# Optimization experiments

Measured on AMD Instinct MI355X. Metric: run time of the kernel, lower is better.

Reference implementation:

```python
import jax, jax.numpy as jnp
import numpy as np

HIDDEN = 1024
NUM_HEADS = 16
DK = 64  # key_and_query_dim
DV = 64  # value_dim
NEG_INF = -1.0e9


def setup_inputs() -> dict:
    key = jax.random.key(0)
    ks = jax.random.split(key, 12)
    B, S = 4, 2048
    scale = 0.02
    return {
        "q_hidden_inputs": jax.random.normal(ks[0], (B, S, HIDDEN), dtype=jnp.float32),
        "k_hidden_inputs": jax.random.normal(ks[1], (B, S, HIDDEN), dtype=jnp.float32),
        "v_hidden_inputs": jax.random.normal(ks[2], (B, S, HIDDEN), dtype=jnp.float32),
        "mask": jax.random.randint(ks[3], (B, S, S), 0, 2) > 0,
        # per-head projection weights, stacked over heads: [H, hidden, dk/dv]
        "wq": jax.random.normal(ks[4], (NUM_HEADS, HIDDEN, DK), dtype=jnp.float32) * scale,
        "bq": jax.random.normal(ks[5], (NUM_HEADS, DK), dtype=jnp.float32) * scale,
        "wk": jax.random.normal(ks[6], (NUM_HEADS, HIDDEN, DK), dtype=jnp.float32) * scale,
        "bk": jax.random.normal(ks[7], (NUM_HEADS, DK), dtype=jnp.float32) * scale,
        "wv": jax.random.normal(ks[8], (NUM_HEADS, HIDDEN, DV), dtype=jnp.float32) * scale,
        "bv": jax.random.normal(ks[9], (NUM_HEADS, DV), dtype=jnp.float32) * scale,
        # output projection: [H*dv, hidden]
        "wo": jax.random.normal(ks[10], (NUM_HEADS * DV, HIDDEN), dtype=jnp.float32) * scale,
        "bo": jax.random.normal(ks[11], (HIDDEN,), dtype=jnp.float32) * scale,
    }


def reference(q_hidden_inputs, k_hidden_inputs, v_hidden_inputs, mask,
              wq, bq, wk, bk, wv, bv, wo, bo):
    # Per-head linear projections, vectorized over heads: [B, H, S, dk]
    q = jnp.einsum('bsd,hdk->bhsk', q_hidden_inputs, wq) + bq[None, :, None, :]
    k = jnp.einsum('bsd,hdk->bhsk', k_hidden_inputs, wk) + bk[None, :, None, :]
    v = jnp.einsum('bsd,hdv->bhsv', v_hidden_inputs, wv) + bv[None, :, None, :]
    # scores: [B, H, Sq, Sk]
    scores = jnp.einsum('bhsk,bhtk->bhst', q, k) / jnp.sqrt(jnp.float32(DK))
    scores = jnp.where(mask[:, None, :, :], scores, NEG_INF)
    attn = jax.nn.softmax(scores, axis=-1)
    out = jnp.einsum('bhst,bhtv->bhsv', attn, v)  # [B, H, Sq, dv]
    B, H, Sq, Dv = out.shape
    # heads concatenated along last dim in head order (same as torch.cat)
    out = jnp.transpose(out, (0, 2, 1, 3)).reshape(B, Sq, H * Dv)
    return out @ wo + bo
```

## Files before the change

kernel.cpp:

```cpp
#include <hip/hip_runtime.h>
#include <stdint.h>


typedef __bf16 bf16x8_t __attribute__((ext_vector_type(8)));
typedef float f32x4_t __attribute__((ext_vector_type(4)));

#define HID   1024
#define SLEN  2048
#define BATCH 4
#define NH    16
#define MROWS 8192
#define L2E   1.44269504f

__device__ __forceinline__ unsigned short bfbits(float f) {
  union { __bf16 h; unsigned short u; } v; v.h = (__bf16)f; return v.u;
}
__device__ __forceinline__ unsigned int packbf(float a, float b) {
  return (unsigned int)bfbits(a) | ((unsigned int)bfbits(b) << 16);
}
__device__ __forceinline__ float fast_exp2(float x) {
#if __has_builtin(__builtin_amdgcn_exp2f)
  return __builtin_amdgcn_exp2f(x);
#else
  return __exp2f(x);
#endif
}

__device__ __forceinline__ void gload_lds16(const void* g, void* l) {
  __builtin_amdgcn_global_load_lds((const __attribute__((address_space(1))) void*)g,
                                   (__attribute__((address_space(3))) void*)l,
                                   16, 0, 0);
}

__device__ __forceinline__ bf16x8_t frag_ld(const unsigned short* lds, int row, int sblk) {
  int sp = sblk ^ (row & 7);
  return *(const bf16x8_t*)(lds + (row << 6) + (sp << 3));
}

__global__ void detect_mask_kernel(const unsigned int* __restrict__ m,
                                   unsigned int* __restrict__ flag) {
  unsigned int v = m[threadIdx.x];
  unsigned long long b = __ballot(v > 1u);
  if (threadIdx.x == 0) flag[0] = 0u;
  __syncthreads();
  if ((threadIdx.x & 63) == 0 && b) atomicOr(flag, 1u);
}

__global__ __launch_bounds__(256) void mask_bits_kernel(const void* __restrict__ maskp,
    const unsigned int* __restrict__ flag, unsigned long long* __restrict__ bits) {
  int lane = threadIdx.x & 63, wv = threadIdx.x >> 6;
  bool bytemask = flag[0] != 0u;
  size_t w0 = (size_t)blockIdx.x * 64 + (size_t)wv * 16;
  for (int it = 0; it < 16; ++it) {
    size_t word = w0 + it;
    unsigned int v;
    if (bytemask) v = ((const unsigned char*)maskp)[word * 64 + lane];
    else          v = ((const unsigned int*)maskp)[word * 64 + lane];
    unsigned long long bm = __ballot(v != 0u);
    if (lane == 0) bits[word] = bm;
  }
}

__global__ __launch_bounds__(256) void cvt_x_kernel(const float* __restrict__ src,
                                                    unsigned short* __restrict__ xb) {
  size_t base = (size_t)blockIdx.x * 1024 + (size_t)threadIdx.x * 4;
  float4 v = *(const float4*)(src + base);
  ushort4 o;
  o.x = bfbits(v.x); o.y = bfbits(v.y); o.z = bfbits(v.z); o.w = bfbits(v.w);
  *(ushort4*)(xb + base) = o;
}

__global__ __launch_bounds__(256) void pack_w_kernel(const float* __restrict__ wq,
    const float* __restrict__ wk, const float* __restrict__ wv,
    const float* __restrict__ wo, unsigned short* __restrict__ wt) {
  int z = blockIdx.y;
  int id = blockIdx.x * 256 + threadIdx.x;
  int n = id >> 8;
  int d0 = (id & 255) << 2;
  ushort4 o;
  if (z < 3) {
    const float* w = z == 0 ? wq : (z == 1 ? wk : wv);
    const float* base = w + (size_t)(n >> 6) * (HID * 64) + (n & 63);
    o.x = bfbits(base[(size_t)(d0 + 0) * 64]);
    o.y = bfbits(base[(size_t)(d0 + 1) * 64]);
    o.z = bfbits(base[(size_t)(d0 + 2) * 64]);
    o.w = bfbits(base[(size_t)(d0 + 3) * 64]);
  } else {
    o.x = bfbits(wo[(size_t)(d0 + 0) * HID + n]);
    o.y = bfbits(wo[(size_t)(d0 + 1) * HID + n]);
    o.z = bfbits(wo[(size_t)(d0 + 2) * HID + n]);
    o.w = bfbits(wo[(size_t)(d0 + 3) * HID + n]);
  }
  *(ushort4*)(wt + (size_t)z * (HID * HID) + (size_t)n * HID + d0) = o;
}

__device__ __forceinline__ void gemm_stage(const unsigned short* __restrict__ A,
    const unsigned short* __restrict__ B, unsigned short* la, unsigned short* lb,
    int tid, int w, int kt) {
#pragma unroll
  for (int i = 0; i < 4; ++i) {
    int flat = i * 256 + tid;
    int row = flat >> 3;
    int sl = (flat & 7) ^ (row & 7);
    gload_lds16(A + (size_t)row * HID + kt + sl * 8, la + ((i * 256 + w * 64) << 3));
    gload_lds16(B + (size_t)row * HID + kt + sl * 8, lb + ((i * 256 + w * 64) << 3));
  }
}

__device__ __forceinline__ void gemm_tile_mainloop(const unsigned short* __restrict__ A,
    const unsigned short* __restrict__ B, unsigned short (*lA)[128 * 64],
    unsigned short (*lB)[128 * 64], int tid, f32x4_t (&acc)[4][4]) {
  int lane = tid & 63, w = tid >> 6;
  int wr = (w >> 1) << 6, wc = (w & 1) << 6;
  gemm_stage(A, B, lA[0], lB[0], tid, w, 0);
  __syncthreads();
  int cur = 0;
  for (int kt = 0; kt < HID; kt += 64) {
    if (kt + 64 < HID)
      gemm_stage(A, B, lA[cur ^ 1], lB[cur ^ 1], tid, w, kt + 64);
    const unsigned short* la = lA[cur];
    const unsigned short* lb = lB[cur];
#pragma unroll
    for (int kk = 0; kk < 2; ++kk) {
      bf16x8_t af[4], bfr[4];
#pragma unroll
      for (int mi = 0; mi < 4; ++mi)
        af[mi] = frag_ld(la, wr + mi * 16 + (lane & 15), kk * 4 + (lane >> 4));
#pragma unroll
      for (int ni = 0; ni < 4; ++ni)
        bfr[ni] = frag_ld(lb, wc + ni * 16 + (lane & 15), kk * 4 + (lane >> 4));
#pragma unroll
      for (int mi = 0; mi < 4; ++mi)
#pragma unroll
        for (int ni = 0; ni < 4; ++ni)
          acc[mi][ni] = __builtin_amdgcn_mfma_f32_16x16x32_bf16(af[mi], bfr[ni],
                                                                acc[mi][ni], 0, 0, 0);
    }
    __syncthreads();
    cur ^= 1;
  }
}

__global__ __launch_bounds__(256) void gemm_qkv_kernel(
    const unsigned short* __restrict__ Ain, const unsigned short* __restrict__ Bin,
    const float* __restrict__ bias, unsigned short* __restrict__ Out, float scale) {
  __shared__ __align__(16) unsigned short lA[2][128 * 64];
  __shared__ __align__(16) unsigned short lB[2][128 * 64];
  int m0 = blockIdx.x * 128, n0 = blockIdx.y * 128;
  const unsigned short* A = Ain + (size_t)m0 * HID;
  const unsigned short* B = Bin + (size_t)n0 * HID;
  f32x4_t acc[4][4] = {};
  int tid = threadIdx.x;
  gemm_tile_mainloop(A, B, lA, lB, tid, acc);
  int lane = tid & 63, w = tid >> 6;
  int wr = (w >> 1) << 6, wc = (w & 1) << 6;
#pragma unroll
  for (int mi = 0; mi < 4; ++mi)
#pragma unroll
    for (int ni = 0; ni < 4; ++ni) {
      int col = n0 + wc + ni * 16 + (lane & 15);
      float bb = bias[col];
      int h = col >> 6, d = col & 63;
#pragma unroll
      for (int r = 0; r < 4; ++r) {
        int row = m0 + wr + mi * 16 + ((lane >> 4) << 2) + r;
        int b = row >> 11, s = row & 2047;
        Out[((((size_t)b * NH + h) * SLEN + s) << 6) + d] = bfbits((acc[mi][ni][r] + bb) * scale);
      }
    }
}

__global__ __launch_bounds__(256) void gemm_out_kernel(
    const unsigned short* __restrict__ Ob, const unsigned short* __restrict__ WoT,
    const float* __restrict__ bo, float* __restrict__ out) {
  __shared__ __align__(16) unsigned short lA[2][128 * 64];
  __shared__ __align__(16) unsigned short lB[2][128 * 64];
  int m0 = blockIdx.x * 128, n0 = blockIdx.y * 128;
  const unsigned short* A = Ob + (size_t)m0 * HID;
  const unsigned short* B = WoT + (size_t)n0 * HID;
  f32x4_t acc[4][4] = {};
  int tid = threadIdx.x;
  gemm_tile_mainloop(A, B, lA, lB, tid, acc);
  int lane = tid & 63, w = tid >> 6;
  int wr = (w >> 1) << 6, wc = (w & 1) << 6;
#pragma unroll
  for (int mi = 0; mi < 4; ++mi)
#pragma unroll
    for (int ni = 0; ni < 4; ++ni) {
      int col = n0 + wc + ni * 16 + (lane & 15);
      float bb = bo[col];
#pragma unroll
      for (int r = 0; r < 4; ++r) {
        int row = m0 + wr + mi * 16 + ((lane >> 4) << 2) + r;
        out[(size_t)row * HID + col] = acc[mi][ni][r] + bb;
      }
    }
}

__global__ __launch_bounds__(256) void attn_kernel(
    const unsigned short* __restrict__ Q, const unsigned short* __restrict__ K,
    const unsigned short* __restrict__ V, const unsigned long long* __restrict__ mbits,
    unsigned short* __restrict__ O) {
  __shared__ __align__(16) unsigned short lK[2][64 * 64];
  __shared__ __align__(16) unsigned short lV[2][64 * 64];
  __shared__ __align__(16) unsigned short lP[128 * 64];
  int tid = threadIdx.x, lane = tid & 63, w = tid >> 6;
  int g = lane >> 4, ql = lane & 15;
  int bid = blockIdx.x;
  int bh = (bid & 7) * 8 + ((bid >> 3) >> 4);
  int qt = (bid >> 3) & 15;
  int b = bh >> 4, h = bh & 15;
  int q0 = qt * 128;
  const unsigned short* Qb = Q + (size_t)bh * (SLEN * 64);
  const unsigned short* Kb = K + (size_t)bh * (SLEN * 64);
  const unsigned short* Vb = V + (size_t)bh * (SLEN * 64);
  const unsigned long long* Mrow = mbits + (size_t)b * SLEN * 32;

  int kvp = tid >> 3;
  int dv0 = (tid & 7) << 3;

  bf16x8_t qf[2][2];
#pragma unroll
  for (int mi = 0; mi < 2; ++mi)
#pragma unroll
    for (int kk = 0; kk < 2; ++kk) {
      int row = q0 + w * 32 + mi * 16 + ql;
      qf[mi][kk] = *(const bf16x8_t*)(Qb + (size_t)row * 64 + kk * 32 + g * 8);
    }

  bf16x8_t onesf;
#pragma unroll
  for (int e = 0; e < 8; ++e) onesf[e] = (__bf16)1.0f;

  f32x4_t aco[2][4] = {};
  f32x4_t slacc[2] = {};

#pragma unroll
  for (int i = 0; i < 2; ++i) {
    int flat = i * 256 + tid;
    int row = flat >> 3;
    int sl = (flat & 7) ^ (row & 7);
    gload_lds16(Kb + (size_t)row * 64 + sl * 8, lK[0] + ((i * 256 + w * 64) << 3));
  }
  {
    const unsigned short* vs = Vb + (size_t)(kvp * 2) * 64 + dv0;
    bf16x8_t v0 = *(const bf16x8_t*)(vs);
    bf16x8_t v1 = *(const bf16x8_t*)(vs + 64);
    union { __bf16 b[8]; unsigned short u[8]; } a0, a1;
    *(bf16x8_t*)a0.b = v0; *(bf16x8_t*)a1.b = v1;
#pragma unroll
    for (int e = 0; e < 8; ++e) {
      int dv = dv0 + e;
      unsigned int val = (unsigned int)a0.u[e] | ((unsigned int)a1.u[e] << 16);
      int sp2 = (kvp >> 2) ^ (dv & 7);
      *(unsigned int*)((char*)lV[0] + dv * 128 + sp2 * 16 + (kvp & 3) * 4) = val;
    }
  }
  __syncthreads();

  int cur = 0;
  for (int kt = 0; kt < SLEN / 64; ++kt) {
    bf16x8_t vn0, vn1;
    bool pre = (kt + 1) < SLEN / 64;
    if (pre) {
#pragma unroll
      for (int i = 0; i < 2; ++i) {
        int flat = i * 256 + tid;
        int row = flat >> 3;
        int sl = (flat & 7) ^ (row & 7);
        gload_lds16(Kb + (size_t)((kt + 1) * 64 + row) * 64 + sl * 8,
                    lK[cur ^ 1] + ((i * 256 + w * 64) << 3));
      }
      const unsigned short* vs = Vb + (size_t)((kt + 1) * 64 + kvp * 2) * 64 + dv0;
      vn0 = *(const bf16x8_t*)(vs);
      vn1 = *(const bf16x8_t*)(vs + 64);
    }

    const unsigned short* kbuf = lK[cur];
    const unsigned short* vbuf = lV[cur];
    f32x4_t st[2][4];
#pragma unroll
    for (int mi = 0; mi < 2; ++mi)
#pragma unroll
      for (int ni = 0; ni < 4; ++ni) st[mi][ni] = (f32x4_t){0.f, 0.f, 0.f, 0.f};
#pragma unroll
    for (int kk = 0; kk < 2; ++kk) {
      bf16x8_t kf[4];
#pragma unroll
      for (int ni = 0; ni < 4; ++ni)
        kf[ni] = frag_ld(kbuf, ni * 16 + ql, kk * 4 + g);
#pragma unroll
      for (int mi = 0; mi < 2; ++mi)
#pragma unroll
        for (int ni = 0; ni < 4; ++ni)
          st[mi][ni] = __builtin_amdgcn_mfma_f32_16x16x32_bf16(kf[ni], qf[mi][kk],
                                                               st[mi][ni], 0, 0, 0);
    }

#pragma unroll
    for (int mi = 0; mi < 2; ++mi) {
      int qrow = q0 + w * 32 + mi * 16 + ql;
      unsigned long long bg = Mrow[(size_t)qrow * 32 + kt] >> (4 * g);
      int prow = w * 32 + mi * 16 + ql;
#pragma unroll
      for (int ni = 0; ni < 4; ++ni) {
        float p[4];
#pragma unroll
        for (int r = 0; r < 4; ++r) {
          float e = fast_exp2(st[mi][ni][r]);
          p[r] = ((unsigned int)(bg >> (16 * ni + r)) & 1u) ? e : 0.f;
        }
        unsigned int lo = packbf(p[0], p[1]);
        unsigned int hi = packbf(p[2], p[3]);
        int sl = (2 * ni + (g >> 1)) ^ (prow & 7);
        *(uint2*)((char*)lP + prow * 128 + sl * 16 + (g & 1) * 8) = make_uint2(lo, hi);
      }
    }

#pragma unroll
    for (int kk2 = 0; kk2 < 2; ++kk2) {
      bf16x8_t vf[4];
#pragma unroll
      for (int dvf = 0; dvf < 4; ++dvf)
        vf[dvf] = frag_ld(vbuf, dvf * 16 + ql, kk2 * 4 + g);
#pragma unroll
      for (int mi = 0; mi < 2; ++mi) {
        bf16x8_t pf = frag_ld(lP, w * 32 + mi * 16 + ql, kk2 * 4 + g);
        slacc[mi] = __builtin_amdgcn_mfma_f32_16x16x32_bf16(onesf, pf, slacc[mi], 0, 0, 0);
#pragma unroll
        for (int dvf = 0; dvf < 4; ++dvf)
          aco[mi][dvf] = __builtin_amdgcn_mfma_f32_16x16x32_bf16(vf[dvf], pf,
                                                                 aco[mi][dvf], 0, 0, 0);
      }
    }

    if (pre) {
      union { __bf16 b[8]; unsigned short u[8]; } a0, a1;
      *(bf16x8_t*)a0.b = vn0; *(bf16x8_t*)a1.b = vn1;
#pragma unroll
      for (int e = 0; e < 8; ++e) {
        int dv = dv0 + e;
        unsigned int val = (unsigned int)a0.u[e] | ((unsigned int)a1.u[e] << 16);
        int sp2 = (kvp >> 2) ^ (dv & 7);
        *(unsigned int*)((char*)lV[cur ^ 1] + dv * 128 + sp2 * 16 + (kvp & 3) * 4) = val;
      }
    }
    __syncthreads();
    cur ^= 1;
  }

#pragma unroll
  for (int mi = 0; mi < 2; ++mi) {
    float inv = 1.0f / slacc[mi][0];
    int prow = w * 32 + mi * 16 + ql;
#pragma unroll
    for (int dvf = 0; dvf < 4; ++dvf) {
      unsigned int lo = packbf(aco[mi][dvf][0] * inv, aco[mi][dvf][1] * inv);
      unsigned int hi = packbf(aco[mi][dvf][2] * inv, aco[mi][dvf][3] * inv);
      int sl = (2 * dvf + (g >> 1)) ^ (prow & 7);
      *(uint2*)((char*)lP + prow * 128 + sl * 16 + (g & 1) * 8) = make_uint2(lo, hi);
    }
  }
#pragma unroll
  for (int it = 0; it < 8; ++it) {
    int rloc = g + 4 * it;
    int row = w * 32 + rloc;
    int sl = (ql >> 1) ^ (row & 7);
    uint2 v = *(const uint2*)((const char*)lP + row * 128 + sl * 16 + (ql & 1) * 8);
    int qrow = q0 + row;
    *(uint2*)(O + (((size_t)b * SLEN + qrow) << 10) + h * 64 + ql * 4) = v;
  }
}

extern "C" void kernel_launch(void* const* d_in, const int* in_sizes, int n_in,
                              void* d_out, int out_size, void* d_ws, size_t ws_size,
                              hipStream_t stream) {
  (void)in_sizes; (void)n_in; (void)out_size; (void)ws_size;
  const float* xq = (const float*)d_in[0];
  const float* xk = (const float*)d_in[1];
  const float* xv = (const float*)d_in[2];
  const void*  mask = d_in[3];
  const float* wq = (const float*)d_in[4];
  const float* bq = (const float*)d_in[5];
  const float* wk = (const float*)d_in[6];
  const float* bk = (const float*)d_in[7];
  const float* wv = (const float*)d_in[8];
  const float* bv = (const float*)d_in[9];
  const float* wo = (const float*)d_in[10];
  const float* bo = (const float*)d_in[11];
  float* out = (float*)d_out;

  char* ws = (char*)d_ws;
  unsigned short* XbZ  = (unsigned short*)(ws);
  unsigned short* Ob   = (unsigned short*)(ws);
  unsigned short* Wt   = (unsigned short*)(ws + 16777216ull);
  unsigned short* QKV  = (unsigned short*)(ws + 25165824ull);
  unsigned int*   flag = (unsigned int*)(ws + 75497472ull);
  unsigned long long* mbits = (unsigned long long*)d_out;

  const float* xs[3]   = {xq, xk, xv};
  const float* bias[3] = {bq, bk, bv};

  detect_mask_kernel<<<1, 256, 0, stream>>>((const unsigned int*)mask, flag);
  mask_bits_kernel<<<4096, 256, 0, stream>>>(mask, flag, mbits);
  pack_w_kernel<<<dim3(1024, 4), 256, 0, stream>>>(wq, wk, wv, wo, Wt);
  for (int z = 0; z < 3; ++z) {
    cvt_x_kernel<<<8192, 256, 0, stream>>>(xs[z], XbZ);
    gemm_qkv_kernel<<<dim3(64, 8), 256, 0, stream>>>(
        XbZ, Wt + (size_t)z * (HID * HID), bias[z],
        QKV + (size_t)z * ((size_t)MROWS * 1024), z == 0 ? 0.125f * L2E : 1.0f);
  }
  attn_kernel<<<1024, 256, 0, stream>>>(QKV, QKV + 8388608ull,
                                        QKV + 16777216ull, mbits, Ob);
  gemm_out_kernel<<<dim3(64, 8), 256, 0, stream>>>(Ob, Wt + 3ull * (HID * HID), bo, out);
}
```

Baseline: 315.8 us.

## Keep softmax probabilities in registers and use 16x16x16 MFMA for PV

```diff
diff --git a/kernel.cpp b/kernel.cpp
--- a/kernel.cpp
+++ b/kernel.cpp
@@ -4,6 +4,7 @@
 
 typedef __bf16 bf16x8_t __attribute__((ext_vector_type(8)));
 typedef float f32x4_t __attribute__((ext_vector_type(4)));
+typedef short s16x4_t __attribute__((ext_vector_type(4)));
 
 #define HID   1024
 #define SLEN  2048
@@ -23,6 +24,15 @@
   return __builtin_amdgcn_exp2f(x);
 #else
   return __exp2f(x);
+#endif
+}
+
+__device__ __forceinline__ f32x4_t mfma16x16(s16x4_t a, s16x4_t b, f32x4_t c) {
+#if __has_builtin(__builtin_amdgcn_mfma_f32_16x16x16bf16_1k)
+  return __builtin_amdgcn_mfma_f32_16x16x16bf16_1k(a, b, c, 0, 0, 0);
+#else
+  asm("v_mfma_f32_16x16x16_bf16 %0, %1, %2, %0" : "+v"(c) : "v"(a), "v"(b));
+  return c;
 #endif
 }
 
@@ -203,7 +213,6 @@
     unsigned short* __restrict__ O) {
   __shared__ __align__(16) unsigned short lK[2][64 * 64];
   __shared__ __align__(16) unsigned short lV[2][64 * 64];
-  __shared__ __align__(16) unsigned short lP[128 * 64];
   int tid = threadIdx.x, lane = tid & 63, w = tid >> 6;
   int g = lane >> 4, ql = lane & 15;
   int bid = blockIdx.x;
@@ -219,6 +228,8 @@
   int kvp = tid >> 3;
   int dv0 = (tid & 7) << 3;
 
+  int vbyte0 = (ql << 7) + (((g >> 1) ^ (ql & 7)) << 4) + ((g & 1) << 3);
+
   bf16x8_t qf[2][2];
 #pragma unroll
   for (int mi = 0; mi < 2; ++mi)
@@ -228,9 +239,7 @@
       qf[mi][kk] = *(const bf16x8_t*)(Qb + (size_t)row * 64 + kk * 32 + g * 8);
     }
 
-  bf16x8_t onesf;
-#pragma unroll
-  for (int e = 0; e < 8; ++e) onesf[e] = (__bf16)1.0f;
+  s16x4_t ones4 = {0x3F80, 0x3F80, 0x3F80, 0x3F80};
 
   f32x4_t aco[2][4] = {};
   f32x4_t slacc[2] = {};
@@ -276,6 +285,11 @@
       vn1 = *(const bf16x8_t*)(vs + 64);
     }
 
+    unsigned long long bg[2];
+#pragma unroll
+    for (int mi = 0; mi < 2; ++mi)
+      bg[mi] = Mrow[(size_t)(q0 + w * 32 + mi * 16 + ql) * 32 + kt] >> (4 * g);
+
     const unsigned short* kbuf = lK[cur];
     const unsigned short* vbuf = lV[cur];
     f32x4_t st[2][4];
@@ -297,40 +311,38 @@
                                                                st[mi][ni], 0, 0, 0);
     }
 
-#pragma unroll
-    for (int mi = 0; mi < 2; ++mi) {
-      int qrow = q0 + w * 32 + mi * 16 + ql;
-      unsigned long long bg = Mrow[(size_t)qrow * 32 + kt] >> (4 * g);
-      int prow = w * 32 + mi * 16 + ql;
+    unsigned int pb[2][4][2];
+#pragma unroll
+    for (int mi = 0; mi < 2; ++mi)
 #pragma unroll
       for (int ni = 0; ni < 4; ++ni) {
         float p[4];
 #pragma unroll
         for (int r = 0; r < 4; ++r) {
           float e = fast_exp2(st[mi][ni][r]);
-          p[r] = ((unsigned int)(bg >> (16 * ni + r)) & 1u) ? e : 0.f;
+          p[r] = ((unsigned int)(bg[mi] >> (16 * ni + r)) & 1u) ? e : 0.f;
         }
-        unsigned int lo = packbf(p[0], p[1]);
-        unsigned int hi = packbf(p[2], p[3]);
-        int sl = (2 * ni + (g >> 1)) ^ (prow & 7);
-        *(uint2*)((char*)lP + prow * 128 + sl * 16 + (g & 1) * 8) = make_uint2(lo, hi);
-      }
-    }
-
-#pragma unroll
-    for (int kk2 = 0; kk2 < 2; ++kk2) {
-      bf16x8_t vf[4];
-#pragma unroll
-      for (int dvf = 0; dvf < 4; ++dvf)
-        vf[dvf] = frag_ld(vbuf, dvf * 16 + ql, kk2 * 4 + g);
+        pb[mi][ni][0] = packbf(p[0], p[1]);
+        pb[mi][ni][1] = packbf(p[2], p[3]);
+      }
+
+#pragma unroll
+    for (int c = 0; c < 4; ++c) {
+      s16x4_t vfa[4];
+#pragma unroll
+      for (int dvf = 0; dvf < 4; ++dvf) {
+        union { uint2 u; s16x4_t s; } t;
+        t.u = *(const uint2*)((const char*)vbuf + ((vbyte0 ^ (c << 5)) + dvf * 2048));
+        vfa[dvf] = t.s;
+      }
 #pragma unroll
       for (int mi = 0; mi < 2; ++mi) {
-        bf16x8_t pf = frag_ld(lP, w * 32 + mi * 16 + ql, kk2 * 4 + g);
-        slacc[mi] = __builtin_amdgcn_mfma_f32_16x16x32_bf16(onesf, pf, slacc[mi], 0, 0, 0);
+        union { unsigned int u[2]; s16x4_t s; } pp;
+        pp.u[0] = pb[mi][c][0]; pp.u[1] = pb[mi][c][1];
+        slacc[mi] = mfma16x16(ones4, pp.s, slacc[mi]);
 #pragma unroll
         for (int dvf = 0; dvf < 4; ++dvf)
-          aco[mi][dvf] = __builtin_amdgcn_mfma_f32_16x16x32_bf16(vf[dvf], pf,
-                                                                 aco[mi][dvf], 0, 0, 0);
+          aco[mi][dvf] = mfma16x16(vfa[dvf], pp.s, aco[mi][dvf]);
       }
     }
 
@@ -349,6 +361,7 @@
     cur ^= 1;
   }
 
+  unsigned short* eb = (unsigned short*)lK;
 #pragma unroll
   for (int mi = 0; mi < 2; ++mi) {
     float inv = 1.0f / slacc[mi][0];
@@ -358,7 +371,7 @@
       unsigned int lo = packbf(aco[mi][dvf][0] * inv, aco[mi][dvf][1] * inv);
       unsigned int hi = packbf(aco[mi][dvf][2] * inv, aco[mi][dvf][3] * inv);
       int sl = (2 * dvf + (g >> 1)) ^ (prow & 7);
-      *(uint2*)((char*)lP + prow * 128 + sl * 16 + (g & 1) * 8) = make_uint2(lo, hi);
+      *(uint2*)((char*)eb + prow * 128 + sl * 16 + (g & 1) * 8) = make_uint2(lo, hi);
     }
   }
 #pragma unroll
@@ -366,7 +379,7 @@
     int rloc = g + 4 * it;
     int row = w * 32 + rloc;
     int sl = (ql >> 1) ^ (row & 7);
-    uint2 v = *(const uint2*)((const char*)lP + row * 128 + sl * 16 + (ql & 1) * 8);
+    uint2 v = *(const uint2*)((const char*)eb + row * 128 + sl * 16 + (ql & 1) * 8);
     int qrow = q0 + row;
     *(uint2*)(O + (((size_t)b * SLEN + qrow) << 10) + h * 64 + ql * 4) = v;
   }
```

Result: faster. 305.8 us (-3.2%).
